# Performance work log

Hardware: AMD Instinct MI355X
Metric: run time of the kernel (lower is better)

The kernel has to match this reference:

```python
import jax, jax.numpy as jnp
import numpy as np

BN_EPS = 1e-5

def conv3d(x, w, b):
    # standard 3D conv, stride 1, pad 1, NCDHW
    out = jax.lax.conv_general_dilated(x, w, (1, 1, 1), ((1, 1), (1, 1), (1, 1)),
                                       dimension_numbers=('NCDHW', 'OIDHW', 'NCDHW'))
    return out + b[None, :, None, None, None]

def batchnorm(x, gamma, beta):
    # training-mode BN over (B, D, H, W) per channel
    mu = x.mean(axis=(0, 2, 3, 4), keepdims=True)
    var = x.var(axis=(0, 2, 3, 4), keepdims=True)
    g = gamma[None, :, None, None, None]
    b = beta[None, :, None, None, None]
    return g * (x - mu) * jax.lax.rsqrt(var + BN_EPS) + b

def deform_conv3d(x, offset, weight, cpg):
    # x: [B,C,D,H,W]; offset: [B, G*27*3, D,H,W] with layout [B,G,27,(d,h,w),D,H,W]
    # weight: [C_out, C_in, 3,3,3]; kernel 3, stride 1, pad 1 -> same spatial size
    B, C, D, H, W = x.shape
    G = C // cpg
    off = offset.reshape(B, G, 27, 3, D, H, W)
    k = jnp.arange(27)
    kd = (k // 9 - 1).astype(x.dtype).reshape(1, 1, 27, 1, 1, 1)
    kh = ((k // 3) % 3 - 1).astype(x.dtype).reshape(1, 1, 27, 1, 1, 1)
    kw = (k % 3 - 1).astype(x.dtype).reshape(1, 1, 27, 1, 1, 1)
    gd = jnp.arange(D, dtype=x.dtype).reshape(1, 1, 1, D, 1, 1)
    gh = jnp.arange(H, dtype=x.dtype).reshape(1, 1, 1, 1, H, 1)
    gw = jnp.arange(W, dtype=x.dtype).reshape(1, 1, 1, 1, 1, W)
    # fractional sampling positions per (batch, group, tap, voxel): [B,G,27,D,H,W]
    pd = gd + kd + off[:, :, :, 0]
    ph = gh + kh + off[:, :, :, 1]
    pw = gw + kw + off[:, :, :, 2]
    d0 = jnp.floor(pd); h0 = jnp.floor(ph); w0 = jnp.floor(pw)
    fd = pd - d0; fh = ph - h0; fw = pw - w0
    d0i = d0.astype(jnp.int32); h0i = h0.astype(jnp.int32); w0i = w0.astype(jnp.int32)
    xg = x.reshape(B, G, cpg, D * H * W)
    N = 27 * D * H * W
    acc = jnp.zeros((B, G, cpg, 27, D, H, W), x.dtype)
    for dd in (0, 1):
        for hh in (0, 1):
            for ww in (0, 1):
                di = d0i + dd; hi = h0i + hh; wi = w0i + ww
                wgt = ((fd if dd else 1.0 - fd) * (fh if hh else 1.0 - fh)
                       * (fw if ww else 1.0 - fw))
                valid = ((di >= 0) & (di < D) & (hi >= 0) & (hi < H)
                         & (wi >= 0) & (wi < W))  # zero padding outside
                dic = jnp.clip(di, 0, D - 1)
                hic = jnp.clip(hi, 0, H - 1)
                wic = jnp.clip(wi, 0, W - 1)
                idx = ((dic * H + hic) * W + wic).reshape(B, G, 1, N)
                vals = jnp.take_along_axis(xg, jnp.broadcast_to(idx, (B, G, cpg, N)), axis=3)
                vals = vals.reshape(B, G, cpg, 27, D, H, W)
                acc = acc + (wgt * valid)[:, :, None] * vals
    wr = weight.reshape(weight.shape[0], G, cpg, 27)
    return jnp.einsum('bgckdhw,ogck->bodhw', acc, wr)

def setup_inputs() -> dict:
    key = jax.random.key(0)
    ks = jax.random.split(key, 8)
    B, C, D, H, W = 2, 64, 8, 32, 32
    cpg = 8
    Coff = (C // cpg) * 3 * 27  # 648
    fan = 1.0 / np.sqrt(C * 27)
    x = jax.random.normal(ks[0], (B, C, D, H, W), jnp.float32)
    w_off1 = jax.random.normal(ks[1], (Coff, C, 3, 3, 3), jnp.float32) * 0.01
    b_off1 = jnp.zeros((Coff,), jnp.float32)
    w1 = jax.random.normal(ks[2], (C, C, 3, 3, 3), jnp.float32) * fan
    g1 = jnp.ones((C,), jnp.float32)
    be1 = jnp.zeros((C,), jnp.float32)
    w_off2 = jax.random.normal(ks[3], (Coff, C, 3, 3, 3), jnp.float32) * 0.01
    b_off2 = jnp.zeros((Coff,), jnp.float32)
    w2 = jax.random.normal(ks[4], (C, C, 3, 3, 3), jnp.float32) * fan
    g2 = jnp.ones((C,), jnp.float32)
    be2 = jnp.zeros((C,), jnp.float32)
    return {'x': x, 'w_off1': w_off1, 'b_off1': b_off1, 'w1': w1, 'g1': g1,
            'be1': be1, 'w_off2': w_off2, 'b_off2': b_off2, 'w2': w2,
            'g2': g2, 'be2': be2, 'cpg': cpg}

def reference(x, w_off1, b_off1, w1, g1, be1, w_off2, b_off2, w2, g2, be2, cpg):
    off1 = conv3d(x, w_off1, b_off1)
    out = deform_conv3d(x, off1, w1, cpg)
    out = jax.nn.relu(batchnorm(out, g1, be1))
    off2 = conv3d(x, w_off2, b_off2)  # note: offsets computed from x, as in source
    out = deform_conv3d(out, off2, w2, cpg)
    out = batchnorm(out, g2, be2) + x
    out = jax.nn.relu(out)
    return (out, off1, off2)
```

## Files before the change

### kernel.cpp

```cpp
#include <hip/hip_runtime.h>
#include <stdint.h>

typedef unsigned short u16;
typedef __attribute__((ext_vector_type(8))) short bf16x8;
typedef __attribute__((ext_vector_type(4))) float f32x4;

#define DEV static __device__ __forceinline__

#define BB    2
#define CC    64
#define DDD   8
#define HHH   32
#define WWW   32
#define DHW   8192
#define MTOT  16384
#define GG    8
#define KTOT  1728
#define NOFF  1296
#define NOFFP 1408
#define COFF  648

#define OFF1_ELEM (BB*CC*DHW)
#define OFF2_ELEM (OFF1_ELEM + BB*COFF*DHW)

#define XCL_OFF   0ull
#define YCL_OFF   2097152ull
#define WOFF_OFF  4194304ull
#define W1_OFF    9060352ull
#define W2_OFF    9281536ull
#define C1_OFF    9502720ull
#define C2_OFF    13697024ull
#define ST1_OFF   17891328ull
#define ST2_OFF   17891840ull
#define ZPG_OFF   17892352ull
#define PART_OFF  17892608ull

DEV float bf2f(u16 u){ union { uint32_t i; float f; } v; v.i = ((uint32_t)u) << 16; return v.f; }
DEV u16 f2bf(float f){ union { float f; uint32_t i; } v; v.f = f;
  uint32_t r = v.i + 0x7fffu + ((v.i >> 16) & 1u); return (u16)(r >> 16); }

DEV void gld16(const void* g, void* l){
  __builtin_amdgcn_global_load_lds((const __attribute__((address_space(1))) void*)g,
                                   (__attribute__((address_space(3))) void*)l, 16, 0, 0);
}

#define PRE0 (BB*CC*DHW)
#define PRE1 (PRE0 + NOFFP*KTOT)
#define PRE2 (PRE1 + CC*KTOT)
#define PRE3 (PRE2 + CC*KTOT)
#define PRETOT (PRE3 + 128)

__global__ void k_prep(const float* __restrict__ x,
                       const float* __restrict__ wo1, const float* __restrict__ wo2,
                       const float* __restrict__ w1, const float* __restrict__ w2,
                       u16* __restrict__ xcl, u16* __restrict__ woff,
                       u16* __restrict__ w1b, u16* __restrict__ w2b,
                       u16* __restrict__ zpg)
{
  int idx = blockIdx.x * 256 + threadIdx.x;
  if (idx < PRE0) {
    int p = idx & (DHW - 1);
    int c = (idx >> 13) & 63;
    int b = idx >> 19;
    xcl[(size_t)(b * DHW + p) * CC + c] = f2bf(x[idx]);
  } else if (idx < PRE1) {
    int j = idx - PRE0;
    int k = j % KTOT, n = j / KTOT;
    int tap = k >> 6, cin = k & 63;
    float v = 0.f;
    if (n < NOFF) {
      const float* w = (n < COFF) ? wo1 : wo2;
      int nn = (n < COFF) ? n : n - COFF;
      v = w[(size_t)nn * KTOT + cin * 27 + tap];
    }
    woff[j] = f2bf(v);
  } else if (idx < PRE2) {
    int j = idx - PRE1;
    int k = j % KTOT, n = j / KTOT;
    int tap = k >> 6, cin = k & 63;
    w1b[j] = f2bf(w1[(size_t)n * KTOT + cin * 27 + tap]);
  } else if (idx < PRE3) {
    int j = idx - PRE2;
    int k = j % KTOT, n = j / KTOT;
    int tap = k >> 6, cin = k & 63;
    w2b[j] = f2bf(w2[(size_t)n * KTOT + cin * 27 + tap]);
  } else if (idx < PRETOT) {
    zpg[idx - PRE3] = 0;
  }
}

__global__ __launch_bounds__(256) void k_gemm_off(
    const u16* __restrict__ xcl, const u16* __restrict__ woff,
    const float* __restrict__ boff1, const float* __restrict__ boff2,
    float* __restrict__ dout, const u16* __restrict__ zpg)
{
  __shared__ u16 Al[128 * 64];
  __shared__ u16 Bl[128 * 64];
  const int tid = threadIdx.x;
  const int wv = tid >> 6, lane = tid & 63;
  const int m0 = blockIdx.x * 128;
  const int n0 = blockIdx.y * 128;
  const int lr = lane >> 3, lc = lane & 7;
  const int lcs = (lc ^ lr) << 3;
  const int b  = m0 >> 13;
  const int p0 = m0 & (DHW - 1);
  int ad[4], ah[4], aw[4];
  #pragma unroll
  for (int i = 0; i < 4; ++i) {
    int p = p0 + wv * 32 + i * 8 + lr;
    ad[i] = p >> 10; ah[i] = (p >> 5) & 31; aw[i] = p & 31;
  }
  const size_t xb = (size_t)b * DHW * CC;

  f32x4 acc[4][4] = {};
  const int wm = wv >> 1, wn = wv & 1;
  const int r16 = lane & 15, q = lane >> 4;
  const int rs = r16 & 7;

  for (int t = 0; t < 27; ++t) {
    int kd = t / 9 - 1, kh = (t / 3) % 3 - 1, kw = t % 3 - 1;
    #pragma unroll
    for (int i = 0; i < 4; ++i) {
      int d2 = ad[i] + kd, h2 = ah[i] + kh, w2 = aw[i] + kw;
      bool ok = ((unsigned)d2 < DDD) & ((unsigned)h2 < HHH) & ((unsigned)w2 < WWW);
      const u16* src = ok ? (xcl + xb + (size_t)((d2 << 10) + (h2 << 5) + w2) * CC + lcs)
                          : zpg;
      gld16(src, &Al[(wv * 32 + i * 8) * 64]);
    }
    #pragma unroll
    for (int i = 0; i < 4; ++i) {
      int r = wv * 32 + i * 8 + lr;
      const u16* src = woff + (size_t)(n0 + r) * KTOT + t * 64 + lcs;
      gld16(src, &Bl[(wv * 32 + i * 8) * 64]);
    }
    __syncthreads();
    #pragma unroll
    for (int kk = 0; kk < 2; ++kk) {
      const int cs = ((kk * 4 + q) ^ rs) << 3;
      bf16x8 af[4], bfr[4];
      #pragma unroll
      for (int i = 0; i < 4; ++i)
        af[i] = *(const bf16x8*)&Al[(wm * 64 + i * 16 + r16) * 64 + cs];
      #pragma unroll
      for (int j = 0; j < 4; ++j)
        bfr[j] = *(const bf16x8*)&Bl[(wn * 64 + j * 16 + r16) * 64 + cs];
      #pragma unroll
      for (int i = 0; i < 4; ++i)
        #pragma unroll
        for (int j = 0; j < 4; ++j)
          acc[i][j] = __builtin_amdgcn_mfma_f32_16x16x32_bf16(af[i], bfr[j], acc[i][j], 0, 0, 0);
    }
    __syncthreads();
  }

  float biasj[4]; int ncj[4];
  #pragma unroll
  for (int j = 0; j < 4; ++j) {
    int nc = n0 + wn * 64 + j * 16 + r16;
    ncj[j] = nc;
    biasj[j] = (nc < NOFF) ? ((nc < COFF) ? boff1[nc] : boff2[nc - COFF]) : 0.f;
  }
  #pragma unroll
  for (int i = 0; i < 4; ++i) {
    int mrow = m0 + wm * 64 + i * 16 + q * 4;
    int bb = mrow >> 13, p = mrow & (DHW - 1);
    #pragma unroll
    for (int j = 0; j < 4; ++j) {
      int nc = ncj[j];
      if (nc < NOFF) {
        int ch = (nc < COFF) ? nc : nc - COFF;
        size_t base = (nc < COFF) ? (size_t)OFF1_ELEM : (size_t)OFF2_ELEM;
        f32x4 v = acc[i][j] + biasj[j];
        *(f32x4*)(dout + base + ((size_t)(bb * COFF + ch)) * DHW + p) = v;
      }
    }
  }
}

__global__ __launch_bounds__(256) void k_deform(
    const u16* __restrict__ src, const float* __restrict__ offs,
    const u16* __restrict__ wB, float* __restrict__ cdst,
    const u16* __restrict__ zpg)
{
  __shared__ u16 Al[2 * 16 * 64];
  __shared__ u16 Bl[2 * 64 * 64];
  const int tid = threadIdx.x;
  const int wv = tid >> 6, lane = tid & 63;
  const int mrow0 = blockIdx.x * 16;
  const int b  = mrow0 >> 13;
  const int p0 = mrow0 & (DHW - 1);

  const int th = tid >> 7;
  const int pl = (tid >> 3) & 15;
  const int g  = tid & 7;
  const int p  = p0 + pl;
  const int d = p >> 10, h = (p >> 5) & 31, w = p & 31;
  const u16* sb = src + (size_t)b * DHW * CC + g * 8;
  const size_t obase = ((size_t)(b * COFF + g * 81)) * DHW + p;
  u16* awp = &Al[th * 1024 + pl * 64 + ((g ^ (pl & 7)) << 3)];

  const int lr = lane >> 3, lc = lane & 7;
  const int lcs = (lc ^ lr) << 3;

  f32x4 acc = {};
  const int r16 = lane & 15, q = lane >> 4;
  const int rs = r16 & 7;

  for (int ph = 0; ph < 14; ++ph) {
    #pragma unroll
    for (int i = 0; i < 4; ++i) {
      int tb = 2 * ph + (i >> 1);
      int row = (i & 1) * 32 + wv * 8 + lr;
      const u16* s = (tb < 27) ? (wB + (size_t)row * KTOT + tb * 64 + lcs) : zpg;
      gld16(s, &Bl[(i >> 1) * 4096 + (((i & 1) * 32 + wv * 8) * 64)]);
    }
    {
      int t = 2 * ph + th;
      float a8[8] = {0.f,0.f,0.f,0.f,0.f,0.f,0.f,0.f};
      if (t < 27) {
        int kd = t / 9 - 1, kh = (t / 3) % 3 - 1, kw = t % 3 - 1;
        size_t ob = obase + (size_t)(t * 3) * DHW;
        float pd = (float)(d + kd) + offs[ob];
        float phh = (float)(h + kh) + offs[ob + DHW];
        float pw = (float)(w + kw) + offs[ob + 2 * DHW];
        float fd0 = floorf(pd), fh0 = floorf(phh), fw0 = floorf(pw);
        float fd = pd - fd0, fh = phh - fh0, fw = pw - fw0;
        int d0 = (int)fd0, h0 = (int)fh0, w0 = (int)fw0;
        #pragma unroll
        for (int dd = 0; dd < 2; ++dd) {
          float wd = dd ? fd : 1.f - fd;
          int di = d0 + dd;
          #pragma unroll
          for (int hh = 0; hh < 2; ++hh) {
            float wh = hh ? fh : 1.f - fh;
            int hi = h0 + hh;
            #pragma unroll
            for (int ww = 0; ww < 2; ++ww) {
              int wi = w0 + ww;
              if (((unsigned)di < DDD) && ((unsigned)hi < HHH) && ((unsigned)wi < WWW)) {
                float wgt = wd * wh * (ww ? fw : 1.f - fw);
                bf16x8 v = *(const bf16x8*)(sb + (size_t)((di << 10) + (hi << 5) + wi) * CC);
                #pragma unroll
                for (int c = 0; c < 8; ++c) a8[c] += wgt * bf2f((u16)v[c]);
              }
            }
          }
        }
      }
      union { bf16x8 v; u16 u[8]; } o;
      #pragma unroll
      for (int c = 0; c < 8; ++c) o.u[c] = f2bf(a8[c]);
      *(bf16x8*)awp = o.v;
    }
    __syncthreads();
    #pragma unroll
    for (int tt = 0; tt < 2; ++tt) {
      #pragma unroll
      for (int kk = 0; kk < 2; ++kk) {
        const int cs = ((kk * 4 + q) ^ rs) << 3;
        bf16x8 af = *(const bf16x8*)&Al[tt * 1024 + r16 * 64 + cs];
        bf16x8 bf_ = *(const bf16x8*)&Bl[tt * 4096 + (wv * 16 + r16) * 64 + cs];
        acc = __builtin_amdgcn_mfma_f32_16x16x32_bf16(af, bf_, acc, 0, 0, 0);
      }
    }
    __syncthreads();
  }

  {
    int nc = wv * 16 + r16;
    int mr = mrow0 + q * 4;
    #pragma unroll
    for (int r = 0; r < 4; ++r)
      cdst[(size_t)(mr + r) * CC + nc] = acc[r];
  }
}

__global__ void k_bnpart(const float* __restrict__ c, float* __restrict__ part)
{
  int k = blockIdx.x, tid = threadIdx.x;
  int ch = tid & 63, sub = tid >> 6;
  float s = 0.f, s2 = 0.f;
  for (int mm = sub; mm < 64; mm += 4) {
    float v = c[(size_t)(k * 64 + mm) * CC + ch];
    s += v; s2 += v * v;
  }
  __shared__ float sh[4][128];
  sh[sub][ch] = s; sh[sub][64 + ch] = s2;
  __syncthreads();
  if (tid < 128)
    part[(size_t)k * 128 + tid] = sh[0][tid] + sh[1][tid] + sh[2][tid] + sh[3][tid];
}

__global__ void k_bnfin(const float* __restrict__ part, const float* __restrict__ gamma,
                        const float* __restrict__ beta, float* __restrict__ stats)
{
  int tid = threadIdx.x;
  float S = 0.f;
  for (int k = 0; k < 256; ++k) S += part[(size_t)k * 128 + tid];
  __shared__ float sh[128];
  sh[tid] = S;
  __syncthreads();
  if (tid < 64) {
    float mu = sh[tid] / (float)MTOT;
    float var = sh[64 + tid] / (float)MTOT - mu * mu;
    float sc = gamma[tid] / sqrtf(var + 1e-5f);
    stats[tid] = sc;
    stats[64 + tid] = beta[tid] - mu * sc;
  }
}

__global__ void k_apply1(const float* __restrict__ c1, const float* __restrict__ st,
                         u16* __restrict__ ycl)
{
  int idx = blockIdx.x * 256 + threadIdx.x;
  if (idx >= MTOT * CC) return;
  int n = idx & 63;
  float v = st[n] * c1[idx] + st[64 + n];
  ycl[idx] = f2bf(fmaxf(v, 0.f));
}

__global__ void k_apply2(const float* __restrict__ c2, const float* __restrict__ st,
                         const float* __restrict__ x, float* __restrict__ out)
{
  int idx = blockIdx.x * 256 + threadIdx.x;
  if (idx >= BB * CC * DHW) return;
  int p = idx & (DHW - 1);
  int n = (idx >> 13) & 63;
  int b = idx >> 19;
  float v = st[n] * c2[(size_t)(b * DHW + p) * CC + n] + st[64 + n] + x[idx];
  out[idx] = fmaxf(v, 0.f);
}

extern "C" void kernel_launch(void* const* d_in, const int* in_sizes, int n_in,
                              void* d_out, int out_size, void* d_ws, size_t ws_size,
                              hipStream_t stream)
{
  (void)in_sizes; (void)n_in; (void)out_size; (void)ws_size;
  const float* x      = (const float*)d_in[0];
  const float* w_off1 = (const float*)d_in[1];
  const float* b_off1 = (const float*)d_in[2];
  const float* w1     = (const float*)d_in[3];
  const float* g1     = (const float*)d_in[4];
  const float* be1    = (const float*)d_in[5];
  const float* w_off2 = (const float*)d_in[6];
  const float* b_off2 = (const float*)d_in[7];
  const float* w2     = (const float*)d_in[8];
  const float* g2     = (const float*)d_in[9];
  const float* be2    = (const float*)d_in[10];

  char* ws = (char*)d_ws;
  u16*   xcl  = (u16*)(ws + XCL_OFF);
  u16*   ycl  = (u16*)(ws + YCL_OFF);
  u16*   woff = (u16*)(ws + WOFF_OFF);
  u16*   w1b  = (u16*)(ws + W1_OFF);
  u16*   w2b  = (u16*)(ws + W2_OFF);
  float* c1   = (float*)(ws + C1_OFF);
  float* c2   = (float*)(ws + C2_OFF);
  float* st1  = (float*)(ws + ST1_OFF);
  float* st2  = (float*)(ws + ST2_OFF);
  u16*   zpg  = (u16*)(ws + ZPG_OFF);
  float* part = (float*)(ws + PART_OFF);
  float* out  = (float*)d_out;

  k_prep<<<(PRETOT + 255) / 256, 256, 0, stream>>>(
      x, w_off1, w_off2, w1, w2, xcl, woff, w1b, w2b, zpg);

  k_gemm_off<<<dim3(MTOT / 128, NOFFP / 128), 256, 0, stream>>>(
      xcl, woff, b_off1, b_off2, out, zpg);

  k_deform<<<MTOT / 16, 256, 0, stream>>>(xcl, out + OFF1_ELEM, w1b, c1, zpg);
  k_bnpart<<<256, 256, 0, stream>>>(c1, part);
  k_bnfin<<<1, 128, 0, stream>>>(part, g1, be1, st1);
  k_apply1<<<(MTOT * CC) / 256, 256, 0, stream>>>(c1, st1, ycl);

  k_deform<<<MTOT / 16, 256, 0, stream>>>(ycl, out + OFF2_ELEM, w2b, c2, zpg);
  k_bnpart<<<256, 256, 0, stream>>>(c2, part);
  k_bnfin<<<1, 128, 0, stream>>>(part, g2, be2, st2);
  k_apply2<<<(BB*CC*DHW) / 256, 256, 0, stream>>>(c2, st2, x, out);
}
```

Baseline: 250.6 us.

## Double-buffer offset GEMM tiles and fuse BN partial sums into deform epilogue

The offset-conv GEMM now uses two LDS buffers. The next tap's global-to-LDS loads are issued before the MFMAs on the current tap, with explicit waitcnt and barriers and raised wave priority during the math. This is meant to hide load latency behind compute. The separate k_bnpart kernel is removed: each deform block reduces per-channel sum and sum-of-squares from its accumulators with shuffles and writes partials. That saves a full re-read of the conv output and one launch, but k_bnfin must now serially reduce four times as many partial rows, and the partial buffer grows, which may exceed the workspace slot it was sized for.

```diff
diff --git a/kernel.cpp b/kernel.cpp
--- a/kernel.cpp
+++ b/kernel.cpp
@@ -94,8 +94,8 @@
     const float* __restrict__ boff1, const float* __restrict__ boff2,
     float* __restrict__ dout, const u16* __restrict__ zpg)
 {
-  __shared__ u16 Al[128 * 64];
-  __shared__ u16 Bl[128 * 64];
+  __shared__ u16 Al[2 * 128 * 64];
+  __shared__ u16 Bl[2 * 128 * 64];
   const int tid = threadIdx.x;
   const int wv = tid >> 6, lane = tid & 63;
   const int m0 = blockIdx.x * 128;
@@ -117,40 +117,60 @@
   const int r16 = lane & 15, q = lane >> 4;
   const int rs = r16 & 7;
 
-  for (int t = 0; t < 27; ++t) {
+  auto stage = [&](int buf, int t) {
     int kd = t / 9 - 1, kh = (t / 3) % 3 - 1, kw = t % 3 - 1;
+    u16* Ab = &Al[buf * 8192];
+    u16* Bb = &Bl[buf * 8192];
     #pragma unroll
     for (int i = 0; i < 4; ++i) {
       int d2 = ad[i] + kd, h2 = ah[i] + kh, w2 = aw[i] + kw;
       bool ok = ((unsigned)d2 < DDD) & ((unsigned)h2 < HHH) & ((unsigned)w2 < WWW);
       const u16* src = ok ? (xcl + xb + (size_t)((d2 << 10) + (h2 << 5) + w2) * CC + lcs)
                           : zpg;
-      gld16(src, &Al[(wv * 32 + i * 8) * 64]);
+      gld16(src, &Ab[(wv * 32 + i * 8) * 64]);
     }
     #pragma unroll
     for (int i = 0; i < 4; ++i) {
       int r = wv * 32 + i * 8 + lr;
       const u16* src = woff + (size_t)(n0 + r) * KTOT + t * 64 + lcs;
-      gld16(src, &Bl[(wv * 32 + i * 8) * 64]);
-    }
-    __syncthreads();
+      gld16(src, &Bb[(wv * 32 + i * 8) * 64]);
+    }
+  };
+
+  stage(0, 0);
+  asm volatile("s_waitcnt vmcnt(0)" ::: "memory");
+  __builtin_amdgcn_sched_barrier(0);
+  __builtin_amdgcn_s_barrier();
+  __builtin_amdgcn_sched_barrier(0);
+
+  int cur = 0;
+  for (int t = 0; t < 27; ++t) {
+    if (t < 26) stage(cur ^ 1, t + 1);
+    const u16* Ab = &Al[cur * 8192];
+    const u16* Bb = &Bl[cur * 8192];
+    __builtin_amdgcn_s_setprio(1);
     #pragma unroll
     for (int kk = 0; kk < 2; ++kk) {
       const int cs = ((kk * 4 + q) ^ rs) << 3;
       bf16x8 af[4], bfr[4];
       #pragma unroll
       for (int i = 0; i < 4; ++i)
-        af[i] = *(const bf16x8*)&Al[(wm * 64 + i * 16 + r16) * 64 + cs];
+        af[i] = *(const bf16x8*)&Ab[(wm * 64 + i * 16 + r16) * 64 + cs];
       #pragma unroll
       for (int j = 0; j < 4; ++j)
-        bfr[j] = *(const bf16x8*)&Bl[(wn * 64 + j * 16 + r16) * 64 + cs];
+        bfr[j] = *(const bf16x8*)&Bb[(wn * 64 + j * 16 + r16) * 64 + cs];
       #pragma unroll
       for (int i = 0; i < 4; ++i)
         #pragma unroll
         for (int j = 0; j < 4; ++j)
           acc[i][j] = __builtin_amdgcn_mfma_f32_16x16x32_bf16(af[i], bfr[j], acc[i][j], 0, 0, 0);
     }
-    __syncthreads();
+    __builtin_amdgcn_s_setprio(0);
+    asm volatile("s_waitcnt vmcnt(0) lgkmcnt(0)" ::: "memory");
+    __builtin_amdgcn_sched_barrier(0);
+    __builtin_amdgcn_s_barrier();
+    __builtin_amdgcn_sched_barrier(0);
+    cur ^= 1;
   }
 
   float biasj[4]; int ncj[4];
@@ -180,7 +200,7 @@
 __global__ __launch_bounds__(256) void k_deform(
     const u16* __restrict__ src, const float* __restrict__ offs,
     const u16* __restrict__ wB, float* __restrict__ cdst,
-    const u16* __restrict__ zpg)
+    const u16* __restrict__ zpg, float* __restrict__ part)
 {
   __shared__ u16 Al[2 * 16 * 64];
   __shared__ u16 Bl[2 * 64 * 64];
@@ -273,22 +293,17 @@
     for (int r = 0; r < 4; ++r)
       cdst[(size_t)(mr + r) * CC + nc] = acc[r];
   }
-}
-
-__global__ void k_bnpart(const float* __restrict__ c, float* __restrict__ part)
-{
-  int k = blockIdx.x, tid = threadIdx.x;
-  int ch = tid & 63, sub = tid >> 6;
-  float s = 0.f, s2 = 0.f;
-  for (int mm = sub; mm < 64; mm += 4) {
-    float v = c[(size_t)(k * 64 + mm) * CC + ch];
-    s += v; s2 += v * v;
-  }
-  __shared__ float sh[4][128];
-  sh[sub][ch] = s; sh[sub][64 + ch] = s2;
-  __syncthreads();
-  if (tid < 128)
-    part[(size_t)k * 128 + tid] = sh[0][tid] + sh[1][tid] + sh[2][tid] + sh[3][tid];
+
+  {
+    float s  = acc[0] + acc[1] + acc[2] + acc[3];
+    float s2 = acc[0]*acc[0] + acc[1]*acc[1] + acc[2]*acc[2] + acc[3]*acc[3];
+    s  += __shfl_down(s, 16, 64);  s  += __shfl_down(s, 32, 64);
+    s2 += __shfl_down(s2, 16, 64); s2 += __shfl_down(s2, 32, 64);
+    if (lane < 16) {
+      part[(size_t)blockIdx.x * 128 + wv * 16 + lane] = s;
+      part[(size_t)blockIdx.x * 128 + 64 + wv * 16 + lane] = s2;
+    }
+  }
 }
 
 __global__ void k_bnfin(const float* __restrict__ part, const float* __restrict__ gamma,
@@ -296,7 +311,8 @@
 {
   int tid = threadIdx.x;
   float S = 0.f;
-  for (int k = 0; k < 256; ++k) S += part[(size_t)k * 128 + tid];
+  #pragma unroll 8
+  for (int k = 0; k < 1024; ++k) S += part[(size_t)k * 128 + tid];
   __shared__ float sh[128];
   sh[tid] = S;
   __syncthreads();
@@ -368,13 +384,11 @@
   k_gemm_off<<<dim3(MTOT / 128, NOFFP / 128), 256, 0, stream>>>(
       xcl, woff, b_off1, b_off2, out, zpg);
 
-  k_deform<<<MTOT / 16, 256, 0, stream>>>(xcl, out + OFF1_ELEM, w1b, c1, zpg);
-  k_bnpart<<<256, 256, 0, stream>>>(c1, part);
+  k_deform<<<MTOT / 16, 256, 0, stream>>>(xcl, out + OFF1_ELEM, w1b, c1, zpg, part);
   k_bnfin<<<1, 128, 0, stream>>>(part, g1, be1, st1);
   k_apply1<<<(MTOT * CC) / 256, 256, 0, stream>>>(c1, st1, ycl);
 
-  k_deform<<<MTOT / 16, 256, 0, stream>>>(ycl, out + OFF2_ELEM, w2b, c2, zpg);
-  k_bnpart<<<256, 256, 0, stream>>>(c2, part);
+  k_deform<<<MTOT / 16, 256, 0, stream>>>(ycl, out + OFF2_ELEM, w2b, c2, zpg, part);
   k_bnfin<<<1, 128, 0, stream>>>(part, g2, be2, st2);
   k_apply2<<<(BB*CC*DHW) / 256, 256, 0, stream>>>(c2, st2, x, out);
 }
```

After: 326.1 us. 30.1% more time.
